# Kernel optimization log

Hardware: AMD Instinct MI355X
Metric: run time of the kernel (lower is better)

The kernel has to match this reference:

```python
import jax, jax.numpy as jnp
import numpy as np

EPS = 1e-8

def _cos(a, b):
    # a: [B,1,d], b: [B,C,d] -> [B,C]  (torch.nn.CosineSimilarity(dim=2) semantics, eps=1e-8)
    na = jnp.maximum(jnp.sqrt(jnp.sum(a * a, axis=-1)), EPS)
    nb = jnp.maximum(jnp.sqrt(jnp.sum(b * b, axis=-1)), EPS)
    return jnp.sum(a * b, axis=-1) / (na * nb)

def setup_inputs() -> dict:
    key = jax.random.key(0)
    ks = jax.random.split(key, 20)
    B, C = 2048, 64
    BERT, CTRY, CODE, MIX = 768, 24, 8, 24
    N_CODES, N_COUNTRIES, GAZ = 654, 250, 9
    s = 0.02
    inp = {
        "placename_tensor": jax.random.normal(ks[0], (B, BERT), jnp.float32),
        "other_locs_tensor": jax.random.normal(ks[1], (B, BERT), jnp.float32),
        "doc_tensor": jax.random.normal(ks[2], (B, BERT), jnp.float32),
        "feature_codes": jax.random.randint(ks[3], (B, C), 0, N_CODES, jnp.int64 if jax.config.jax_enable_x64 else jnp.int32),
        "country_codes": jax.random.randint(ks[4], (B, C), 0, N_COUNTRIES, jnp.int64 if jax.config.jax_enable_x64 else jnp.int32),
        "gaz_info": jax.random.normal(ks[5], (B, C, GAZ), jnp.float32),
        # learned params
        "code_emb_table": jax.random.normal(ks[6], (N_CODES, CODE), jnp.float32),
        "country_emb_table": jax.random.normal(ks[7], (N_COUNTRIES, BERT), jnp.float32),
        "W_cet": jax.random.normal(ks[8], (CTRY, BERT), jnp.float32) * s,
        "b_cet": jnp.zeros((CTRY,), jnp.float32),
        "W_t2c": jax.random.normal(ks[9], (CTRY, BERT), jnp.float32) * s,
        "b_t2c": jnp.zeros((CTRY,), jnp.float32),
        "W_ctx": jax.random.normal(ks[10], (CTRY, BERT), jnp.float32) * s,
        "b_ctx": jnp.zeros((CTRY,), jnp.float32),
        "W_code": jax.random.normal(ks[11], (CODE, BERT), jnp.float32) * s,
        "b_code": jnp.zeros((CODE,), jnp.float32),
        "W_mix1": jax.random.normal(ks[12], (MIX, 13), jnp.float32) * 0.2,
        "b_mix1": jnp.zeros((MIX,), jnp.float32),
        "W_mix2": jax.random.normal(ks[13], (MIX, MIX), jnp.float32) * 0.2,
        "b_mix2": jnp.zeros((MIX,), jnp.float32),
        "W_last": jax.random.normal(ks[14], (1, MIX), jnp.float32) * 0.2,
        "b_last": jnp.zeros((1,), jnp.float32),
    }
    return inp

def reference(placename_tensor, other_locs_tensor, doc_tensor, feature_codes, country_codes,
              gaz_info, code_emb_table, country_emb_table, W_cet, b_cet, W_t2c, b_t2c,
              W_ctx, b_ctx, W_code, b_code, W_mix1, b_mix1, W_mix2, b_mix2, W_last, b_last):
    # eval mode: dropout = identity
    x = placename_tensor @ W_t2c.T + b_t2c            # [B,24]
    x_code = placename_tensor @ W_code.T + b_code     # [B,8]
    x_other = other_locs_tensor @ W_ctx.T + b_ctx     # [B,24]
    x_doc = doc_tensor @ W_ctx.T + b_ctx              # [B,24]
    fc = code_emb_table[feature_codes]                # [B,C,8]
    cc = country_emb_table[country_codes] @ W_cet.T + b_cet  # [B,C,24]
    sim_country = _cos(x[:, None, :], cc)             # [B,C]
    sim_code = _cos(x_code[:, None, :], fc)
    sim_other = _cos(x_other[:, None, :], cc)
    sim_doc = _cos(x_doc[:, None, :], cc)
    both = jnp.concatenate([sim_country[..., None], sim_code[..., None],
                            sim_other[..., None], sim_doc[..., None], gaz_info], axis=2)  # [B,C,13]
    h = jax.nn.sigmoid(both @ W_mix1.T + b_mix1)
    h = jax.nn.sigmoid(h @ W_mix2.T + b_mix2)
    last = jnp.squeeze(h @ W_last.T + b_last, axis=2)  # [B,C]
    return jax.nn.softmax(last, axis=1)
```

## Files before the change

### kernel.cpp

```cpp
#include <hip/hip_runtime.h>
#include <math.h>

#define BB 2048
#define CC 64
#define BERT 768
#define N_CTRY 250
#define N_CODES 654

#define OFF_PCHAT   0
#define OFF_CODEHAT (250*24)
#define OFF_XALL    (OFF_CODEHAT + 654*8)
#define OFF_SSQ     (OFF_XALL + 2048*80)

#define RPB 8
#define ROWGRPS (BB / RPB)
#define PROJ_BLOCKS (5 * ROWGRPS)

__global__ __launch_bounds__(256) void k_proj(
    const float* __restrict__ place, const float* __restrict__ other,
    const float* __restrict__ doc,
    const float* __restrict__ W_t2c, const float* __restrict__ b_t2c,
    const float* __restrict__ W_code, const float* __restrict__ b_code,
    const float* __restrict__ W_ctx, const float* __restrict__ b_ctx,
    const float* __restrict__ ctab, const float* __restrict__ W_cet,
    const float* __restrict__ b_cet, const float* __restrict__ code_emb,
    float* __restrict__ ws) {
  __shared__ float s_ss[RPB][4];
  __shared__ float s_p24[24];
  __shared__ float s_inv1;

  const int bid = blockIdx.x;
  const int tid = threadIdx.x;
  const int w = tid >> 6, lane = tid & 63;

  if (bid < PROJ_BLOCKS) {
    float* xall = ws + OFF_XALL;
    float* ssq  = ws + OFF_SSQ;
    const int cb = bid / ROWGRPS;
    const int rg = bid % ROWGRPS;
    const int row0 = rg * RPB;
    const int j0 = cb * 16 + w * 4;
    const float* wbase; const float* xbase; const float* bbase; int jb;
    if (j0 < 24)      { wbase = W_t2c;  bbase = b_t2c;  jb = j0;      xbase = place; }
    else if (j0 < 32) { wbase = W_code; bbase = b_code; jb = j0 - 24; xbase = place; }
    else if (j0 < 56) { wbase = W_ctx;  bbase = b_ctx;  jb = j0 - 32; xbase = other; }
    else              { wbase = W_ctx;  bbase = b_ctx;  jb = j0 - 56; xbase = doc;   }
    const int jsub = lane & 3, kq = lane >> 2;
    const float bias = bbase[jb + jsub];

    float4 wv[12];
    {
      const float4* wr = (const float4*)(wbase + (size_t)(jb + jsub) * BERT);
#pragma unroll
      for (int i = 0; i < 12; ++i) wv[i] = wr[kq + 16 * i];
    }

    float acc[RPB];
#pragma unroll
    for (int r = 0; r < RPB; ++r) {
      const float4* xr = (const float4*)(xbase + (size_t)(row0 + r) * BERT);
      float s0 = 0.f, s1 = 0.f, s2 = 0.f, s3 = 0.f;
#pragma unroll
      for (int i = 0; i < 12; i += 4) {
        float4 a0 = xr[kq + 16 * (i + 0)];
        float4 a1 = xr[kq + 16 * (i + 1)];
        float4 a2 = xr[kq + 16 * (i + 2)];
        float4 a3 = xr[kq + 16 * (i + 3)];
        s0 += a0.x * wv[i+0].x + a0.y * wv[i+0].y + a0.z * wv[i+0].z + a0.w * wv[i+0].w;
        s1 += a1.x * wv[i+1].x + a1.y * wv[i+1].y + a1.z * wv[i+1].z + a1.w * wv[i+1].w;
        s2 += a2.x * wv[i+2].x + a2.y * wv[i+2].y + a2.z * wv[i+2].z + a2.w * wv[i+2].w;
        s3 += a3.x * wv[i+3].x + a3.y * wv[i+3].y + a3.z * wv[i+3].z + a3.w * wv[i+3].w;
      }
      acc[r] = (s0 + s1) + (s2 + s3);
    }

#pragma unroll
    for (int m = 4; m <= 32; m <<= 1)
#pragma unroll
      for (int r = 0; r < RPB; ++r) acc[r] += __shfl_xor(acc[r], m, 64);

    float v2[RPB];
#pragma unroll
    for (int r = 0; r < RPB; ++r) {
      const float val = acc[r] + bias;
      if (kq == 0) xall[(size_t)(row0 + r) * 80 + j0 + jsub] = val;
      v2[r] = val * val;
    }
#pragma unroll
    for (int r = 0; r < RPB; ++r) v2[r] += __shfl_xor(v2[r], 1, 64);
#pragma unroll
    for (int r = 0; r < RPB; ++r) v2[r] += __shfl_xor(v2[r], 2, 64);
    if (lane == 0) {
#pragma unroll
      for (int r = 0; r < RPB; ++r) s_ss[r][w] = v2[r];
    }
    __syncthreads();
    if (tid < RPB * 2) {
      const int r = tid >> 1, s = tid & 1;
      ssq[(size_t)(row0 + r) * 10 + cb * 2 + s] = s_ss[r][2 * s] + s_ss[r][2 * s + 1];
    }
  } else if (bid < PROJ_BLOCKS + N_CTRY) {
    float* pchat = ws + OFF_PCHAT;
    const int b = bid - PROJ_BLOCKS;
    float4 xa[3];
#pragma unroll
    for (int i = 0; i < 3; ++i)
      xa[i] = ((const float4*)(ctab + (size_t)b * BERT))[lane + 64 * i];
    float acc6[6];
#pragma unroll
    for (int jj = 0; jj < 6; ++jj) acc6[jj] = 0.f;
#pragma unroll
    for (int jj = 0; jj < 6; ++jj) {
      const int j = w * 6 + jj;
      const float4* wr = (const float4*)(W_cet + (size_t)j * BERT);
#pragma unroll
      for (int i = 0; i < 3; ++i) {
        float4 wvv = wr[lane + 64 * i];
        acc6[jj] += xa[i].x * wvv.x + xa[i].y * wvv.y + xa[i].z * wvv.z + xa[i].w * wvv.w;
      }
    }
#pragma unroll
    for (int s = 32; s >= 1; s >>= 1)
#pragma unroll
      for (int jj = 0; jj < 6; ++jj) acc6[jj] += __shfl_xor(acc6[jj], s, 64);
    if (lane == 0) {
#pragma unroll
      for (int jj = 0; jj < 6; ++jj) s_p24[w * 6 + jj] = acc6[jj] + b_cet[w * 6 + jj];
    }
    __syncthreads();
    if (tid == 0) {
      float ss = 0.f;
      for (int k = 0; k < 24; ++k) ss += s_p24[k] * s_p24[k];
      s_inv1 = 1.f / fmaxf(sqrtf(ss), 1e-8f);
    }
    __syncthreads();
    if (tid < 24) pchat[b * 24 + tid] = s_p24[tid] * s_inv1;
  } else {
    float* codehat = ws + OFF_CODEHAT;
    const int idx = (bid - PROJ_BLOCKS - N_CTRY) * 256 + tid;
    if (idx < N_CODES) {
      float v[8];
      float ss = 0.f;
#pragma unroll
      for (int k = 0; k < 8; ++k) { v[k] = code_emb[idx * 8 + k]; ss += v[k] * v[k]; }
      const float inv = 1.f / fmaxf(sqrtf(ss), 1e-8f);
#pragma unroll
      for (int k = 0; k < 8; ++k) codehat[idx * 8 + k] = v[k] * inv;
    }
  }
}

__global__ __launch_bounds__(256) void k_classify(
    const int* __restrict__ fcodes, const int* __restrict__ ccodes,
    const float* __restrict__ gaz,
    const float* __restrict__ W_mix1, const float* __restrict__ b_mix1,
    const float* __restrict__ W_mix2, const float* __restrict__ b_mix2,
    const float* __restrict__ W_last, const float* __restrict__ b_last,
    const float* __restrict__ ws, float* __restrict__ out) {
  __shared__ float s_pch[N_CTRY * 25];
  const int tid = threadIdx.x;
  const int w = tid >> 6, lane = tid & 63;
  const int row0 = blockIdx.x * 4;

  {
    const float* pch = ws + OFF_PCHAT;
    for (int e = tid; e < N_CTRY * 24; e += 256)
      s_pch[(e / 24) * 25 + (e % 24)] = pch[e];
  }
  __syncthreads();

  const int row = __builtin_amdgcn_readfirstlane(row0 + w);
  const float* xv = ws + OFF_XALL + (size_t)row * 80;
  const float* q  = ws + OFF_SSQ + (size_t)row * 10;
  const float g0 = q[0] + q[1] + q[2];
  const float g1 = q[3];
  const float g2 = q[4] + q[5] + q[6];
  const float g3 = q[7] + q[8] + q[9];
  const float inv0 = 1.f / fmaxf(sqrtf(g0), 1e-8f);
  const float inv1 = 1.f / fmaxf(sqrtf(g1), 1e-8f);
  const float inv2 = 1.f / fmaxf(sqrtf(g2), 1e-8f);
  const float inv3 = 1.f / fmaxf(sqrtf(g3), 1e-8f);

  const int cidx = ccodes[row * CC + lane];
  const int fidx = fcodes[row * CC + lane];

  float cc[24];
#pragma unroll
  for (int k = 0; k < 24; ++k) cc[k] = s_pch[cidx * 25 + k];
  float cd[8];
  {
    const float4* q4 = (const float4*)(ws + OFF_CODEHAT + fidx * 8);
#pragma unroll
    for (int i = 0; i < 2; ++i) {
      float4 v = q4[i];
      cd[4*i+0] = v.x; cd[4*i+1] = v.y; cd[4*i+2] = v.z; cd[4*i+3] = v.w;
    }
  }

  float sc = 0.f, so = 0.f, sd = 0.f, sq = 0.f;
#pragma unroll
  for (int k = 0; k < 24; ++k) {
    const float ck = cc[k];
    sc += xv[k] * ck;
    so += xv[32 + k] * ck;
    sd += xv[56 + k] * ck;
  }
#pragma unroll
  for (int k = 0; k < 8; ++k) sq += xv[24 + k] * cd[k];

  float f[13];
  f[0] = sc * inv0;
  f[1] = sq * inv1;
  f[2] = so * inv2;
  f[3] = sd * inv3;
  {
    const float* g = gaz + (size_t)(row * CC + lane) * 9;
    float4 ga = ((const float4*)g)[0];
    float4 gb = ((const float4*)g)[1];
    f[4] = ga.x; f[5] = ga.y; f[6] = ga.z; f[7] = ga.w;
    f[8] = gb.x; f[9] = gb.y; f[10] = gb.z; f[11] = gb.w;
    f[12] = g[8];
  }

  float h1[24];
#pragma unroll
  for (int j = 0; j < 24; ++j) {
    float a = b_mix1[j];
#pragma unroll
    for (int i = 0; i < 13; ++i) a += W_mix1[j * 13 + i] * f[i];
    h1[j] = 1.f / (1.f + __expf(-a));
  }
  float h2[24];
#pragma unroll
  for (int j = 0; j < 24; ++j) {
    float a = b_mix2[j];
#pragma unroll
    for (int i = 0; i < 24; ++i) a += W_mix2[j * 24 + i] * h1[i];
    h2[j] = 1.f / (1.f + __expf(-a));
  }
  float last = b_last[0];
#pragma unroll
  for (int k = 0; k < 24; ++k) last += W_last[k] * h2[k];

  float mx = last;
#pragma unroll
  for (int s = 32; s >= 1; s >>= 1) mx = fmaxf(mx, __shfl_xor(mx, s, 64));
  const float e = __expf(last - mx);
  float ssum = e;
#pragma unroll
  for (int s = 32; s >= 1; s >>= 1) ssum += __shfl_xor(ssum, s, 64);
  out[row * CC + lane] = e / ssum;
}

extern "C" void kernel_launch(void* const* d_in, const int* in_sizes, int n_in,
                              void* d_out, int out_size, void* d_ws, size_t ws_size,
                              hipStream_t stream) {
  const float* place   = (const float*)d_in[0];
  const float* other   = (const float*)d_in[1];
  const float* doc     = (const float*)d_in[2];
  const int*   fcodes  = (const int*)d_in[3];
  const int*   ccodes  = (const int*)d_in[4];
  const float* gaz     = (const float*)d_in[5];
  const float* code_emb= (const float*)d_in[6];
  const float* ctab    = (const float*)d_in[7];
  const float* W_cet   = (const float*)d_in[8];
  const float* b_cet   = (const float*)d_in[9];
  const float* W_t2c   = (const float*)d_in[10];
  const float* b_t2c   = (const float*)d_in[11];
  const float* W_ctx   = (const float*)d_in[12];
  const float* b_ctx   = (const float*)d_in[13];
  const float* W_code  = (const float*)d_in[14];
  const float* b_code  = (const float*)d_in[15];
  const float* W_mix1  = (const float*)d_in[16];
  const float* b_mix1  = (const float*)d_in[17];
  const float* W_mix2  = (const float*)d_in[18];
  const float* b_mix2  = (const float*)d_in[19];
  const float* W_last  = (const float*)d_in[20];
  const float* b_last  = (const float*)d_in[21];
  float* ws  = (float*)d_ws;
  float* out = (float*)d_out;

  k_proj<<<PROJ_BLOCKS + N_CTRY + 3, 256, 0, stream>>>(
      place, other, doc, W_t2c, b_t2c, W_code, b_code, W_ctx, b_ctx,
      ctab, W_cet, b_cet, code_emb, ws);
  k_classify<<<BB / 4, 256, 0, stream>>>(fcodes, ccodes, gaz, W_mix1, b_mix1,
                                         W_mix2, b_mix2, W_last, b_last, ws, out);
}
```

Measured before the change: 143.4 us.

## Fuse projection and classify kernels into one persistent kernel with grid barrier

Merges the projection and classification kernels into a single 512-block persistent kernel. Work is split into per-wave tasks that loop over projection, country-table and code-normalize jobs, followed by a global atomic-counter grid barrier before the classify phase. The per-row sum-of-squares is now written per wave instead of reduced through shared memory, and a memset resets the counter each call. This removes one kernel launch gap and the block-level syncs. The cost is an added memset launch and the risk of a spin-barrier deadlock if all 512 blocks are not co-resident.

Result: slower. 294.0 us (+105.0%).

```diff
diff --git a/kernel.cpp b/kernel.cpp
--- a/kernel.cpp
+++ b/kernel.cpp
@@ -8,15 +8,19 @@
 #define N_CODES 654
 
 #define OFF_PCHAT   0
-#define OFF_CODEHAT (250*24)
-#define OFF_XALL    (OFF_CODEHAT + 654*8)
-#define OFF_SSQ     (OFF_XALL + 2048*80)
-
-#define RPB 8
-#define ROWGRPS (BB / RPB)
-#define PROJ_BLOCKS (5 * ROWGRPS)
-
-__global__ __launch_bounds__(256) void k_proj(
+#define OFF_CODEHAT (N_CTRY * 24)
+#define OFF_XALL    (OFF_CODEHAT + N_CODES*8)
+#define OFF_SSQ     (OFF_XALL + BB*80)
+#define OFF_CTR     (OFF_SSQ + BB*20)
+
+#define NBLK   512
+#define NWAVES (NBLK * 4)
+#define RPB    8
+#define TPROJ  5120
+#define TCTRY  (TPROJ + N_CTRY)
+#define NTASK  (TCTRY + 11)
+
+__global__ __launch_bounds__(256) void k_all(
     const float* __restrict__ place, const float* __restrict__ other,
     const float* __restrict__ doc,
     const float* __restrict__ W_t2c, const float* __restrict__ b_t2c,
@@ -24,158 +28,165 @@
     const float* __restrict__ W_ctx, const float* __restrict__ b_ctx,
     const float* __restrict__ ctab, const float* __restrict__ W_cet,
     const float* __restrict__ b_cet, const float* __restrict__ code_emb,
-    float* __restrict__ ws) {
-  __shared__ float s_ss[RPB][4];
-  __shared__ float s_p24[24];
-  __shared__ float s_inv1;
-
-  const int bid = blockIdx.x;
-  const int tid = threadIdx.x;
-  const int w = tid >> 6, lane = tid & 63;
-
-  if (bid < PROJ_BLOCKS) {
-    float* xall = ws + OFF_XALL;
-    float* ssq  = ws + OFF_SSQ;
-    const int cb = bid / ROWGRPS;
-    const int rg = bid % ROWGRPS;
-    const int row0 = rg * RPB;
-    const int j0 = cb * 16 + w * 4;
-    const float* wbase; const float* xbase; const float* bbase; int jb;
-    if (j0 < 24)      { wbase = W_t2c;  bbase = b_t2c;  jb = j0;      xbase = place; }
-    else if (j0 < 32) { wbase = W_code; bbase = b_code; jb = j0 - 24; xbase = place; }
-    else if (j0 < 56) { wbase = W_ctx;  bbase = b_ctx;  jb = j0 - 32; xbase = other; }
-    else              { wbase = W_ctx;  bbase = b_ctx;  jb = j0 - 56; xbase = doc;   }
-    const int jsub = lane & 3, kq = lane >> 2;
-    const float bias = bbase[jb + jsub];
-
-    float4 wv[12];
-    {
-      const float4* wr = (const float4*)(wbase + (size_t)(jb + jsub) * BERT);
-#pragma unroll
-      for (int i = 0; i < 12; ++i) wv[i] = wr[kq + 16 * i];
-    }
-
-    float acc[RPB];
-#pragma unroll
-    for (int r = 0; r < RPB; ++r) {
-      const float4* xr = (const float4*)(xbase + (size_t)(row0 + r) * BERT);
-      float s0 = 0.f, s1 = 0.f, s2 = 0.f, s3 = 0.f;
-#pragma unroll
-      for (int i = 0; i < 12; i += 4) {
-        float4 a0 = xr[kq + 16 * (i + 0)];
-        float4 a1 = xr[kq + 16 * (i + 1)];
-        float4 a2 = xr[kq + 16 * (i + 2)];
-        float4 a3 = xr[kq + 16 * (i + 3)];
-        s0 += a0.x * wv[i+0].x + a0.y * wv[i+0].y + a0.z * wv[i+0].z + a0.w * wv[i+0].w;
-        s1 += a1.x * wv[i+1].x + a1.y * wv[i+1].y + a1.z * wv[i+1].z + a1.w * wv[i+1].w;
-        s2 += a2.x * wv[i+2].x + a2.y * wv[i+2].y + a2.z * wv[i+2].z + a2.w * wv[i+2].w;
-        s3 += a3.x * wv[i+3].x + a3.y * wv[i+3].y + a3.z * wv[i+3].z + a3.w * wv[i+3].w;
-      }
-      acc[r] = (s0 + s1) + (s2 + s3);
-    }
-
-#pragma unroll
-    for (int m = 4; m <= 32; m <<= 1)
-#pragma unroll
-      for (int r = 0; r < RPB; ++r) acc[r] += __shfl_xor(acc[r], m, 64);
-
-    float v2[RPB];
-#pragma unroll
-    for (int r = 0; r < RPB; ++r) {
-      const float val = acc[r] + bias;
-      if (kq == 0) xall[(size_t)(row0 + r) * 80 + j0 + jsub] = val;
-      v2[r] = val * val;
-    }
-#pragma unroll
-    for (int r = 0; r < RPB; ++r) v2[r] += __shfl_xor(v2[r], 1, 64);
-#pragma unroll
-    for (int r = 0; r < RPB; ++r) v2[r] += __shfl_xor(v2[r], 2, 64);
-    if (lane == 0) {
-#pragma unroll
-      for (int r = 0; r < RPB; ++r) s_ss[r][w] = v2[r];
-    }
-    __syncthreads();
-    if (tid < RPB * 2) {
-      const int r = tid >> 1, s = tid & 1;
-      ssq[(size_t)(row0 + r) * 10 + cb * 2 + s] = s_ss[r][2 * s] + s_ss[r][2 * s + 1];
-    }
-  } else if (bid < PROJ_BLOCKS + N_CTRY) {
-    float* pchat = ws + OFF_PCHAT;
-    const int b = bid - PROJ_BLOCKS;
-    float4 xa[3];
-#pragma unroll
-    for (int i = 0; i < 3; ++i)
-      xa[i] = ((const float4*)(ctab + (size_t)b * BERT))[lane + 64 * i];
-    float acc6[6];
-#pragma unroll
-    for (int jj = 0; jj < 6; ++jj) acc6[jj] = 0.f;
-#pragma unroll
-    for (int jj = 0; jj < 6; ++jj) {
-      const int j = w * 6 + jj;
-      const float4* wr = (const float4*)(W_cet + (size_t)j * BERT);
-#pragma unroll
-      for (int i = 0; i < 3; ++i) {
-        float4 wvv = wr[lane + 64 * i];
-        acc6[jj] += xa[i].x * wvv.x + xa[i].y * wvv.y + xa[i].z * wvv.z + xa[i].w * wvv.w;
-      }
-    }
-#pragma unroll
-    for (int s = 32; s >= 1; s >>= 1)
-#pragma unroll
-      for (int jj = 0; jj < 6; ++jj) acc6[jj] += __shfl_xor(acc6[jj], s, 64);
-    if (lane == 0) {
-#pragma unroll
-      for (int jj = 0; jj < 6; ++jj) s_p24[w * 6 + jj] = acc6[jj] + b_cet[w * 6 + jj];
-    }
-    __syncthreads();
-    if (tid == 0) {
-      float ss = 0.f;
-      for (int k = 0; k < 24; ++k) ss += s_p24[k] * s_p24[k];
-      s_inv1 = 1.f / fmaxf(sqrtf(ss), 1e-8f);
-    }
-    __syncthreads();
-    if (tid < 24) pchat[b * 24 + tid] = s_p24[tid] * s_inv1;
-  } else {
-    float* codehat = ws + OFF_CODEHAT;
-    const int idx = (bid - PROJ_BLOCKS - N_CTRY) * 256 + tid;
-    if (idx < N_CODES) {
-      float v[8];
-      float ss = 0.f;
-#pragma unroll
-      for (int k = 0; k < 8; ++k) { v[k] = code_emb[idx * 8 + k]; ss += v[k] * v[k]; }
-      const float inv = 1.f / fmaxf(sqrtf(ss), 1e-8f);
-#pragma unroll
-      for (int k = 0; k < 8; ++k) codehat[idx * 8 + k] = v[k] * inv;
-    }
-  }
-}
-
-__global__ __launch_bounds__(256) void k_classify(
     const int* __restrict__ fcodes, const int* __restrict__ ccodes,
     const float* __restrict__ gaz,
     const float* __restrict__ W_mix1, const float* __restrict__ b_mix1,
     const float* __restrict__ W_mix2, const float* __restrict__ b_mix2,
     const float* __restrict__ W_last, const float* __restrict__ b_last,
-    const float* __restrict__ ws, float* __restrict__ out) {
+    float* __restrict__ ws, float* __restrict__ out) {
   __shared__ float s_pch[N_CTRY * 25];
+
   const int tid = threadIdx.x;
   const int w = tid >> 6, lane = tid & 63;
-  const int row0 = blockIdx.x * 4;
-
-  {
-    const float* pch = ws + OFF_PCHAT;
-    for (int e = tid; e < N_CTRY * 24; e += 256)
-      s_pch[(e / 24) * 25 + (e % 24)] = pch[e];
-  }
+  const int kq = lane >> 2, jsub = lane & 3;
+  const int gw = blockIdx.x * 4 + w;
+
+  float* pchat   = ws + OFF_PCHAT;
+  float* codehat = ws + OFF_CODEHAT;
+  float* xall    = ws + OFF_XALL;
+  float* ssq     = ws + OFF_SSQ;
+
+  for (int t = gw; t < NTASK; t += NWAVES) {
+    if (t < TPROJ) {
+      const int cb = t >> 10;
+      const int rem = t & 1023;
+      const int row0 = (rem >> 2) * RPB;
+      const int jquad = rem & 3;
+      const int j0 = cb * 16 + jquad * 4;
+      const float* wbase; const float* xbase; const float* bbase; int jb;
+      if (j0 < 24)      { wbase = W_t2c;  bbase = b_t2c;  jb = j0;      xbase = place; }
+      else if (j0 < 32) { wbase = W_code; bbase = b_code; jb = j0 - 24; xbase = place; }
+      else if (j0 < 56) { wbase = W_ctx;  bbase = b_ctx;  jb = j0 - 32; xbase = other; }
+      else              { wbase = W_ctx;  bbase = b_ctx;  jb = j0 - 56; xbase = doc;   }
+      const float bias = bbase[jb + jsub];
+
+      float4 wv[12];
+      {
+        const float4* wr = (const float4*)(wbase + (size_t)(jb + jsub) * BERT);
+#pragma unroll
+        for (int i = 0; i < 12; ++i) wv[i] = wr[kq + 16 * i];
+      }
+      float acc[RPB];
+#pragma unroll
+      for (int r = 0; r < RPB; ++r) {
+        const float4* xr = (const float4*)(xbase + (size_t)(row0 + r) * BERT);
+        float s0 = 0.f, s1 = 0.f, s2 = 0.f, s3 = 0.f;
+#pragma unroll
+        for (int i = 0; i < 12; i += 4) {
+          float4 a0 = xr[kq + 16 * (i + 0)];
+          float4 a1 = xr[kq + 16 * (i + 1)];
+          float4 a2 = xr[kq + 16 * (i + 2)];
+          float4 a3 = xr[kq + 16 * (i + 3)];
+          s0 += a0.x*wv[i+0].x + a0.y*wv[i+0].y + a0.z*wv[i+0].z + a0.w*wv[i+0].w;
+          s1 += a1.x*wv[i+1].x + a1.y*wv[i+1].y + a1.z*wv[i+1].z + a1.w*wv[i+1].w;
+          s2 += a2.x*wv[i+2].x + a2.y*wv[i+2].y + a2.z*wv[i+2].z + a2.w*wv[i+2].w;
+          s3 += a3.x*wv[i+3].x + a3.y*wv[i+3].y + a3.z*wv[i+3].z + a3.w*wv[i+3].w;
+        }
+        acc[r] = (s0 + s1) + (s2 + s3);
+      }
+#pragma unroll
+      for (int m = 4; m <= 32; m <<= 1)
+#pragma unroll
+        for (int r = 0; r < RPB; ++r) acc[r] += __shfl_xor(acc[r], m, 64);
+
+      float v2[RPB];
+#pragma unroll
+      for (int r = 0; r < RPB; ++r) {
+        acc[r] += bias;
+        v2[r] = acc[r] * acc[r];
+      }
+      if (kq == 0) {
+#pragma unroll
+        for (int r = 0; r < RPB; ++r)
+          xall[(size_t)(row0 + r) * 80 + j0 + jsub] = acc[r];
+      }
+#pragma unroll
+      for (int r = 0; r < RPB; ++r) v2[r] += __shfl_xor(v2[r], 1, 64);
+#pragma unroll
+      for (int r = 0; r < RPB; ++r) v2[r] += __shfl_xor(v2[r], 2, 64);
+      if (lane == 0) {
+#pragma unroll
+        for (int r = 0; r < RPB; ++r)
+          ssq[(size_t)(row0 + r) * 20 + cb * 4 + jquad] = v2[r];
+      }
+    } else if (t < TCTRY) {
+      const int b = t - TPROJ;
+      const float4* xr = (const float4*)(ctab + (size_t)b * BERT);
+      float4 xa[12];
+#pragma unroll
+      for (int i = 0; i < 12; ++i) xa[i] = xr[kq + 16 * i];
+      float val[6];
+#pragma unroll
+      for (int g = 0; g < 6; ++g) {
+        const int j = 4 * g + jsub;
+        const float4* wr = (const float4*)(W_cet + (size_t)j * BERT);
+        float s0 = 0.f, s1 = 0.f, s2 = 0.f, s3 = 0.f;
+#pragma unroll
+        for (int i = 0; i < 12; i += 4) {
+          float4 w0 = wr[kq + 16 * (i + 0)];
+          float4 w1 = wr[kq + 16 * (i + 1)];
+          float4 w2 = wr[kq + 16 * (i + 2)];
+          float4 w3 = wr[kq + 16 * (i + 3)];
+          s0 += xa[i+0].x*w0.x + xa[i+0].y*w0.y + xa[i+0].z*w0.z + xa[i+0].w*w0.w;
+          s1 += xa[i+1].x*w1.x + xa[i+1].y*w1.y + xa[i+1].z*w1.z + xa[i+1].w*w1.w;
+          s2 += xa[i+2].x*w2.x + xa[i+2].y*w2.y + xa[i+2].z*w2.z + xa[i+2].w*w2.w;
+          s3 += xa[i+3].x*w3.x + xa[i+3].y*w3.y + xa[i+3].z*w3.z + xa[i+3].w*w3.w;
+        }
+        val[g] = (s0 + s1) + (s2 + s3);
+      }
+#pragma unroll
+      for (int m = 4; m <= 32; m <<= 1)
+#pragma unroll
+        for (int g = 0; g < 6; ++g) val[g] += __shfl_xor(val[g], m, 64);
+      float ss = 0.f;
+#pragma unroll
+      for (int g = 0; g < 6; ++g) {
+        val[g] += b_cet[4 * g + jsub];
+        ss += val[g] * val[g];
+      }
+      ss += __shfl_xor(ss, 1, 64);
+      ss += __shfl_xor(ss, 2, 64);
+      const float inv = 1.f / fmaxf(sqrtf(ss), 1e-8f);
+      if (kq == 0) {
+#pragma unroll
+        for (int g = 0; g < 6; ++g) pchat[b * 24 + 4 * g + jsub] = val[g] * inv;
+      }
+    } else {
+      const int idx = (t - TCTRY) * 64 + lane;
+      if (idx < N_CODES) {
+        float v[8];
+        float ss = 0.f;
+#pragma unroll
+        for (int k = 0; k < 8; ++k) { v[k] = code_emb[idx * 8 + k]; ss += v[k] * v[k]; }
+        const float inv = 1.f / fmaxf(sqrtf(ss), 1e-8f);
+#pragma unroll
+        for (int k = 0; k < 8; ++k) codehat[idx * 8 + k] = v[k] * inv;
+      }
+    }
+  }
+
+  __threadfence();
   __syncthreads();
-
-  const int row = __builtin_amdgcn_readfirstlane(row0 + w);
-  const float* xv = ws + OFF_XALL + (size_t)row * 80;
-  const float* q  = ws + OFF_SSQ + (size_t)row * 10;
-  const float g0 = q[0] + q[1] + q[2];
-  const float g1 = q[3];
-  const float g2 = q[4] + q[5] + q[6];
-  const float g3 = q[7] + q[8] + q[9];
+  if (tid == 0) {
+    unsigned* ctr = (unsigned*)(ws + OFF_CTR);
+    atomicAdd(ctr, 1u);
+    while (__hip_atomic_load(ctr, __ATOMIC_ACQUIRE, __HIP_MEMORY_SCOPE_AGENT) < NBLK)
+      __builtin_amdgcn_s_sleep(2);
+  }
+  __syncthreads();
+  __threadfence();
+
+  for (int e = tid; e < N_CTRY * 24; e += 256)
+    s_pch[(e / 24) * 25 + (e % 24)] = pchat[e];
+  __syncthreads();
+
+  const int row = __builtin_amdgcn_readfirstlane(blockIdx.x * 4 + w);
+  const float* xv = xall + (size_t)row * 80;
+  const float* q  = ssq  + (size_t)row * 20;
+  const float g0 = q[0]+q[1]+q[2]+q[3]+q[4]+q[5];
+  const float g1 = q[6]+q[7];
+  const float g2 = q[8]+q[9]+q[10]+q[11]+q[12]+q[13];
+  const float g3 = q[14]+q[15]+q[16]+q[17]+q[18]+q[19];
   const float inv0 = 1.f / fmaxf(sqrtf(g0), 1e-8f);
   const float inv1 = 1.f / fmaxf(sqrtf(g1), 1e-8f);
   const float inv2 = 1.f / fmaxf(sqrtf(g2), 1e-8f);
@@ -189,7 +200,7 @@
   for (int k = 0; k < 24; ++k) cc[k] = s_pch[cidx * 25 + k];
   float cd[8];
   {
-    const float4* q4 = (const float4*)(ws + OFF_CODEHAT + fidx * 8);
+    const float4* q4 = (const float4*)(codehat + fidx * 8);
 #pragma unroll
     for (int i = 0; i < 2; ++i) {
       float4 v = q4[i];
@@ -280,9 +291,9 @@
   float* ws  = (float*)d_ws;
   float* out = (float*)d_out;
 
-  k_proj<<<PROJ_BLOCKS + N_CTRY + 3, 256, 0, stream>>>(
+  hipMemsetAsync((char*)d_ws + (size_t)OFF_CTR * sizeof(float), 0, sizeof(unsigned), stream);
+  k_all<<<NBLK, 256, 0, stream>>>(
       place, other, doc, W_t2c, b_t2c, W_code, b_code, W_ctx, b_ctx,
-      ctab, W_cet, b_cet, code_emb, ws);
-  k_classify<<<BB / 4, 256, 0, stream>>>(fcodes, ccodes, gaz, W_mix1, b_mix1,
-                                         W_mix2, b_mix2, W_last, b_last, ws, out);
+      ctab, W_cet, b_cet, code_emb, fcodes, ccodes, gaz,
+      W_mix1, b_mix1, W_mix2, b_mix2, W_last, b_last, ws, out);
 }
```
